# Optimization experiments

Hardware: AMD Instinct MI355X
Metric: run time of the kernel (lower is better)

The kernel has to match this reference:

```python
import jax, jax.numpy as jnp
import numpy as np

N = 100000   # nodes
E = 1000000  # directed edges (before self-loops)
G = 512      # graphs in the batch
NEG_SLOPE = 0.2
EPS = 1e-5


def setup_inputs() -> dict:
    key = jax.random.key(0)
    ks = jax.random.split(key, 24)
    r = lambda i, shape, s=0.1: (jax.random.normal(ks[i], shape) * s).astype(jnp.float32)
    return {
        'x': jax.random.normal(ks[0], (N, 27), dtype=jnp.float32),
        'edge_index': jax.random.randint(ks[1], (2, E), 0, N, dtype=jnp.int32),
        'batch': jnp.sort(jax.random.randint(ks[2], (N,), 0, G, dtype=jnp.int32)),
        # GATv2Conv(26, 32, heads=2)
        'Wl1': r(3, (26, 64)), 'bl1': jnp.zeros(64, jnp.float32),
        'Wr1': r(4, (26, 64)), 'br1': jnp.zeros(64, jnp.float32),
        'att1': r(5, (2, 32)), 'b1': jnp.zeros(64, jnp.float32),
        'g1': jnp.ones(64, jnp.float32), 'be1': jnp.zeros(64, jnp.float32),
        # GATv2Conv(64, 32, heads=1)
        'Wl2': r(6, (64, 32)), 'bl2': jnp.zeros(32, jnp.float32),
        'Wr2': r(7, (64, 32)), 'br2': jnp.zeros(32, jnp.float32),
        'att2': r(8, (1, 32)), 'b2': jnp.zeros(32, jnp.float32),
        'g2': jnp.ones(32, jnp.float32), 'be2': jnp.zeros(32, jnp.float32),
        # gate_nn: 32 -> 16 -> 1
        'Wg1': r(9, (32, 16)), 'bg1': jnp.zeros(16, jnp.float32),
        'Wg2': r(10, (16, 1)), 'bg2': jnp.zeros(1, jnp.float32),
        # final head: 33 -> 16 -> 1
        'Wh1': r(11, (33, 16)), 'bh1': jnp.zeros(16, jnp.float32),
        'Wh2': r(12, (16, 1)), 'bh2': jnp.zeros(1, jnp.float32),
    }


def _gatv2(x, Wl, bl, Wr, br, att, bias, src, dst, heads, ch):
    n = x.shape[0]
    xl = (x @ Wl + bl).reshape(n, heads, ch)  # source projection (messages)
    xr = (x @ Wr + br).reshape(n, heads, ch)  # target projection
    e = jax.nn.leaky_relu(xl[src] + xr[dst], NEG_SLOPE)      # [Etot, H, C]
    logits = jnp.einsum('ehc,hc->eh', e, att)                 # [Etot, H]
    m = jax.ops.segment_max(logits, dst, num_segments=n)
    a = jnp.exp(logits - m[dst])
    z = jax.ops.segment_sum(a, dst, num_segments=n)
    a = a / (z[dst] + 1e-16)
    out = jax.ops.segment_sum(xl[src] * a[:, :, None], dst, num_segments=n)
    return out.reshape(n, heads * ch) + bias


def _batchnorm(h, gamma, beta):
    mu = h.mean(axis=0)
    var = jnp.var(h, axis=0)  # biased, matches torch normalization
    return (h - mu) * jax.lax.rsqrt(var + EPS) * gamma + beta


def reference(x, edge_index, batch, Wl1, bl1, Wr1, br1, att1, b1, g1, be1,
              Wl2, bl2, Wr2, br2, att2, b2, g2, be2,
              Wg1, bg1, Wg2, bg2, Wh1, bh1, Wh2, bh2):
    n = x.shape[0]
    loops = jnp.arange(n, dtype=edge_index.dtype)
    src = jnp.concatenate([edge_index[0], loops])
    dst = jnp.concatenate([edge_index[1], loops])
    x_no_cost = jnp.concatenate([x[:, :24], x[:, 25:]], axis=1)  # [N, 26]
    h = jax.nn.elu(_batchnorm(_gatv2(x_no_cost, Wl1, bl1, Wr1, br1, att1, b1, src, dst, 2, 32), g1, be1))
    # dropout is identity in eval mode
    h = jax.nn.elu(_batchnorm(_gatv2(h, Wl2, bl2, Wr2, br2, att2, b2, src, dst, 1, 32), g2, be2))
    # attentional aggregation: gate MLP + segment softmax over graphs
    gate = jax.nn.relu(h @ Wg1 + bg1) @ Wg2 + bg2               # [N, 1]
    gm = jax.ops.segment_max(gate, batch, num_segments=G)
    ga = jnp.exp(gate - gm[batch])
    gz = jax.ops.segment_sum(ga, batch, num_segments=G)
    ga = ga / (gz[batch] + 1e-16)
    h_pooled = jax.ops.segment_sum(ga * h, batch, num_segments=G)  # [G, 32]
    counts = jax.ops.segment_sum(jnp.ones((n, 1), x.dtype), batch, num_segments=G)
    root_costs = jax.ops.segment_sum(x[:, 24:25], batch, num_segments=G) / jnp.maximum(counts, 1.0)
    combined = jnp.concatenate([h_pooled, root_costs], axis=1)   # [G, 33]
    return jax.nn.relu(combined @ Wh1 + bh1) @ Wh2 + bh2         # [G, 1]
```

## Files before the change

kernel.cpp:

```cpp
#include <hip/hip_runtime.h>
#include <hip/hip_fp16.h>
#include <math.h>

#define NEG 0.2f
#define BN_EPS 1e-5f
#define BKT_W 256
#define CHUNK 4096


__global__ __launch_bounds__(256)
void hist_kernel(const int* __restrict__ ei, int E, int nbh, int nbkt, int* __restrict__ cnt)
{
    __shared__ int hist[512];
    for (int i = threadIdx.x; i < nbkt; i += 256) hist[i] = 0;
    __syncthreads();
    const int g0 = blockIdx.x * (CHUNK / 4);
    #pragma unroll
    for (int it = 0; it < CHUNK / 1024; ++it) {
        int e = (g0 + it * 256 + threadIdx.x) * 4;
        if (e + 3 < E) {
            int4 d4 = *(const int4*)(ei + E + e);
            atomicAdd(&hist[d4.x >> 8], 1);
            atomicAdd(&hist[d4.y >> 8], 1);
            atomicAdd(&hist[d4.z >> 8], 1);
            atomicAdd(&hist[d4.w >> 8], 1);
        } else {
            for (int k = 0; k < 4; ++k)
                if (e + k < E) atomicAdd(&hist[ei[E + e + k] >> 8], 1);
        }
    }
    __syncthreads();
    for (int i = threadIdx.x; i < nbkt; i += 256) cnt[(size_t)i * nbh + blockIdx.x] = hist[i];
}

__global__ __launch_bounds__(256)
void scan_block_kernel(const int* __restrict__ in, int* __restrict__ out,
                       int* __restrict__ bsum, int n)
{
    __shared__ int s[256];
    int i = blockIdx.x * 256 + threadIdx.x;
    int v = (i < n) ? in[i] : 0;
    s[threadIdx.x] = v;
    __syncthreads();
    for (int off = 1; off < 256; off <<= 1) {
        int t = (threadIdx.x >= off) ? s[threadIdx.x - off] : 0;
        __syncthreads();
        s[threadIdx.x] += t;
        __syncthreads();
    }
    if (i < n) out[i + 1] = s[threadIdx.x];
    if (threadIdx.x == 255) bsum[blockIdx.x] = s[255];
}

__global__ __launch_bounds__(512)
void scan_sums_kernel(int* __restrict__ bsum, int nb)
{
    __shared__ int s[512];
    int v = (threadIdx.x < nb) ? bsum[threadIdx.x] : 0;
    s[threadIdx.x] = v;
    __syncthreads();
    for (int off = 1; off < 512; off <<= 1) {
        int t = (threadIdx.x >= off) ? s[threadIdx.x - off] : 0;
        __syncthreads();
        s[threadIdx.x] += t;
        __syncthreads();
    }
    if (threadIdx.x < nb) bsum[threadIdx.x] = s[threadIdx.x] - v;
}

__global__ __launch_bounds__(256)
void scan_add_kernel(int* __restrict__ out, const int* __restrict__ bsum, int n)
{
    int i = blockIdx.x * 256 + threadIdx.x;
    if (i < n) out[i + 1] += bsum[blockIdx.x];
    if (i == 0) out[0] = 0;
}

__global__ __launch_bounds__(256)
void scat_kernel(const int* __restrict__ ei, int E, int nbh, int nbkt,
                 const int* __restrict__ base, int2* __restrict__ pairs)
{
    __shared__ int fill[512];
    __shared__ int lbase[512];
    for (int i = threadIdx.x; i < nbkt; i += 256) {
        fill[i]  = 0;
        lbase[i] = base[(size_t)i * nbh + blockIdx.x];
    }
    __syncthreads();
    const int g0 = blockIdx.x * (CHUNK / 4);
    #pragma unroll
    for (int it = 0; it < CHUNK / 1024; ++it) {
        int e = (g0 + it * 256 + threadIdx.x) * 4;
        if (e + 3 < E) {
            int4 s4 = *(const int4*)(ei + e);
            int4 d4 = *(const int4*)(ei + E + e);
            int b, r;
            b = d4.x >> 8; r = atomicAdd(&fill[b], 1); pairs[lbase[b] + r] = make_int2(s4.x, d4.x);
            b = d4.y >> 8; r = atomicAdd(&fill[b], 1); pairs[lbase[b] + r] = make_int2(s4.y, d4.y);
            b = d4.z >> 8; r = atomicAdd(&fill[b], 1); pairs[lbase[b] + r] = make_int2(s4.z, d4.z);
            b = d4.w >> 8; r = atomicAdd(&fill[b], 1); pairs[lbase[b] + r] = make_int2(s4.w, d4.w);
        } else {
            for (int k = 0; k < 4; ++k) {
                if (e + k < E) {
                    int s = ei[e + k], d = ei[E + e + k];
                    int b = d >> 8;
                    int r = atomicAdd(&fill[b], 1);
                    pairs[lbase[b] + r] = make_int2(s, d);
                }
            }
        }
    }
}

__global__ __launch_bounds__(256)
void bucket_build_kernel(const int2* __restrict__ pairs, const int* __restrict__ base,
                         int nbh, int nbkt, int n, int E,
                         int* __restrict__ rowptr, int* __restrict__ srcs,
                         int* __restrict__ perm)
{
    const int b     = blockIdx.x;
    const int start = base[(size_t)b * nbh];
    const int end   = base[(size_t)(b + 1) * nbh];
    __shared__ int hist[256], sc[256], dcnt[64], dbase[64];
    hist[threadIdx.x] = 0;
    if (threadIdx.x < 64) dcnt[threadIdx.x] = 0;
    __syncthreads();
    for (int j = start + threadIdx.x; j < end; j += 256)
        atomicAdd(&hist[pairs[j].y & 255], 1);
    __syncthreads();
    const int v = hist[threadIdx.x];
    sc[threadIdx.x] = v;
    __syncthreads();
    for (int off = 1; off < 256; off <<= 1) {
        int t = (threadIdx.x >= off) ? sc[threadIdx.x - off] : 0;
        __syncthreads();
        sc[threadIdx.x] += t;
        __syncthreads();
    }
    const int excl = sc[threadIdx.x] - v;
    const int d = b * 256 + threadIdx.x;
    int bin = 0, rnk = 0;
    if (d < n) {
        rowptr[d] = start + excl;
        bin = min(v, 63);
        rnk = atomicAdd(&dcnt[bin], 1);
    }
    if (b == nbkt - 1 && threadIdx.x == 0) rowptr[n] = E;
    __syncthreads();
    hist[threadIdx.x] = excl;
    __syncthreads();
    for (int j = start + threadIdx.x; j < end; j += 256) {
        int2 p = pairs[j];
        int r = atomicAdd(&hist[p.y & 255], 1);
        srcs[start + r] = p.x;
    }
    if (threadIdx.x < 64) dbase[threadIdx.x] = dcnt[threadIdx.x];
    __syncthreads();
    for (int off = 1; off < 64; off <<= 1) {
        int t = 0;
        if (threadIdx.x < 64 && threadIdx.x >= off) t = dbase[threadIdx.x - off];
        __syncthreads();
        if (threadIdx.x < 64) dbase[threadIdx.x] += t;
        __syncthreads();
    }
    if (d < n) perm[b * 256 + (dbase[bin] - dcnt[bin]) + rnk] = d;
}


__device__ __forceinline__ void gat_step4(const uint2 raw, const float* __restrict__ xrv,
                                          const float* __restrict__ at,
                                          float& z, float* __restrict__ acc)
{
    union { uint2 u; __half2 h[2]; } q; q.u = raw;
    const float2 a = __half22float2(q.h[0]);
    const float2 b = __half22float2(q.h[1]);
    float t, p = 0.f;
    t = a.x + xrv[0]; t = t > 0.f ? t : NEG * t; p += t * at[0];
    t = a.y + xrv[1]; t = t > 0.f ? t : NEG * t; p += t * at[1];
    t = b.x + xrv[2]; t = t > 0.f ? t : NEG * t; p += t * at[2];
    t = b.y + xrv[3]; t = t > 0.f ? t : NEG * t; p += t * at[3];
    p += __shfl_xor(p, 1, 64);
    p += __shfl_xor(p, 2, 64);
    p += __shfl_xor(p, 4, 64);
    const float w = __expf(p);
    z += w;
    acc[0] += w * a.x; acc[1] += w * a.y; acc[2] += w * b.x; acc[3] += w * b.y;
}

template<int HC>
__global__ __launch_bounds__(256)
void gat_fused_kernel(const __half* __restrict__ xl, const float* __restrict__ xr,
                      const float* __restrict__ att,
                      const int* __restrict__ rowptr, const int* __restrict__ srcs,
                      const int* __restrict__ perm,
                      float* __restrict__ outp, int n)
{
    constexpr int LPG = HC / 4;
    const int gid  = (blockIdx.x * 256 + threadIdx.x) / LPG;
    const int lane = threadIdx.x % LPG;
    if (gid >= n) return;
    const int d = perm[gid];

    float at[4], xrv[4];
    {
        const float4 a = *(const float4*)(att + lane * 4);
        at[0] = a.x; at[1] = a.y; at[2] = a.z; at[3] = a.w;
        const float4 x0 = *(const float4*)(xr + (size_t)d * HC + lane * 4);
        xrv[0] = x0.x; xrv[1] = x0.y; xrv[2] = x0.z; xrv[3] = x0.w;
    }

    float z = 0.f, acc[4] = {0.f, 0.f, 0.f, 0.f};
    gat_step4(*(const uint2*)(xl + (size_t)d * HC + lane * 4), xrv, at, z, acc);

    const int jb = rowptr[d], je = rowptr[d + 1];
    int j = jb;
    for (; j + 4 <= je; j += 4) {
        const int s0 = srcs[j], s1 = srcs[j + 1], s2 = srcs[j + 2], s3 = srcs[j + 3];
        const uint2 r0 = *(const uint2*)(xl + (size_t)s0 * HC + lane * 4);
        const uint2 r1 = *(const uint2*)(xl + (size_t)s1 * HC + lane * 4);
        const uint2 r2 = *(const uint2*)(xl + (size_t)s2 * HC + lane * 4);
        const uint2 r3 = *(const uint2*)(xl + (size_t)s3 * HC + lane * 4);
        gat_step4(r0, xrv, at, z, acc);
        gat_step4(r1, xrv, at, z, acc);
        gat_step4(r2, xrv, at, z, acc);
        gat_step4(r3, xrv, at, z, acc);
    }
    for (; j < je; ++j)
        gat_step4(*(const uint2*)(xl + (size_t)srcs[j] * HC + lane * 4), xrv, at, z, acc);

    const float inv = 1.f / (z + 1e-16f);
    *(float4*)(outp + (size_t)d * HC + lane * 4) =
        make_float4(acc[0] * inv, acc[1] * inv, acc[2] * inv, acc[3] * inv);
}

template<int K, int OC, bool DROP24, bool FUSE_NORM>
__global__ __launch_bounds__(256)
void proj_kernel(const float* __restrict__ in, int in_stride,
                 const float* __restrict__ Wl, const float* __restrict__ bl,
                 const float* __restrict__ Wr, const float* __restrict__ br,
                 const float* __restrict__ stats, const float* __restrict__ gamma,
                 const float* __restrict__ beta, float inv_n,
                 __half* __restrict__ outl, float* __restrict__ outr, int n)
{
    constexpr int C2  = 2 * OC;
    constexpr int RPI = 256 / C2;
    __shared__ float Wlds[K][C2];
    __shared__ float xs[RPI][K];
    __shared__ float cs[RPI][OC];

    for (int i = threadIdx.x; i < K * OC; i += 256) {
        int k = i / OC, c = i % OC;
        Wlds[k][c]      = Wl[i];
        Wlds[k][OC + c] = Wr[i];
    }
    float na = 1.f, nb = 0.f;
    if constexpr (FUSE_NORM) {
        int kk  = threadIdx.x % K;
        float mu  = stats[kk] * inv_n;
        float var = stats[K + kk] * inv_n - mu * mu;
        float rs  = rsqrtf(var + BN_EPS) * gamma[kk];
        na = rs; nb = beta[kk] - mu * rs;
    }
    __syncthreads();

    const int col  = threadIdx.x % C2;
    const int rloc = threadIdx.x / C2;
    const int rowBase = blockIdx.x * 8;
    const float bias = (col < OC) ? bl[col] : br[col - OC];

    for (int it = 0; it < 8 / RPI; ++it) {
        int row0 = rowBase + it * RPI;
        __syncthreads();
        for (int i = threadIdx.x; i < RPI * K; i += 256) {
            int rr = i / K, k = i % K;
            int row = row0 + rr;
            float v = 0.f;
            if (row < n) {
                if constexpr (DROP24) {
                    int sc = (k < 24) ? k : k + 1;
                    v = in[(size_t)row * in_stride + sc];
                } else {
                    v = in[(size_t)row * in_stride + k];
                }
                if constexpr (FUSE_NORM) {
                    float t = v * na + nb;
                    v = t > 0.f ? t : expm1f(t);
                }
            }
            xs[rr][k] = v;
        }
        __syncthreads();
        int row = row0 + rloc;
        if (row < n) {
            float acc = bias;
            #pragma unroll
            for (int k = 0; k < K; ++k) acc += xs[rloc][k] * Wlds[k][col];
            if (col < OC) cs[rloc][col] = acc;
            else          outr[(size_t)row * OC + (col - OC)] = acc;
        }
        __syncthreads();
        constexpr int NH2 = RPI * OC / 2;
        if (threadIdx.x < NH2) {
            int rr = threadIdx.x / (OC / 2);
            int c  = threadIdx.x % (OC / 2);
            int row2 = row0 + rr;
            if (row2 < n) {
                __half2 hv = __float22half2_rn(make_float2(cs[rr][2 * c], cs[rr][2 * c + 1]));
                *(__half2*)(outl + (size_t)row2 * OC + 2 * c) = hv;
            }
        }
    }
}

template<int C>
__global__ __launch_bounds__(256)
void bn_stats_kernel(const float* __restrict__ h, int n, float* __restrict__ stats)
{
    constexpr int RPB = 256 / C;
    int col = threadIdx.x % C, rg = threadIdx.x / C;
    float s = 0.f, s2 = 0.f;
    for (int r = blockIdx.x * RPB + rg; r < n; r += gridDim.x * RPB) {
        float v = h[(size_t)r * C + col];
        s += v; s2 += v * v;
    }
    __shared__ float red0[256], red1[256];
    red0[threadIdx.x] = s; red1[threadIdx.x] = s2;
    __syncthreads();
    for (int st = 128; st >= C; st >>= 1) {
        if (threadIdx.x < st) {
            red0[threadIdx.x] += red0[threadIdx.x + st];
            red1[threadIdx.x] += red1[threadIdx.x + st];
        }
        __syncthreads();
    }
    if (threadIdx.x < C) {
        atomicAdd(&stats[threadIdx.x],     red0[threadIdx.x]);
        atomicAdd(&stats[C + threadIdx.x], red1[threadIdx.x]);
    }
}

__global__ __launch_bounds__(256)
void gate_norm_kernel(float* __restrict__ h2, int n,
                      const float* __restrict__ stats, const float* __restrict__ gamma,
                      const float* __restrict__ beta, float inv_n,
                      const float* __restrict__ Wg1, const float* __restrict__ bg1,
                      const float* __restrict__ Wg2, const float* __restrict__ bg2,
                      float* __restrict__ gate)
{
    __shared__ float W1[512], W2[16], B1[16], A_[32], B_[32];
    for (int i = threadIdx.x; i < 512; i += 256) W1[i] = Wg1[i];
    if (threadIdx.x < 16) { W2[threadIdx.x] = Wg2[threadIdx.x]; B1[threadIdx.x] = bg1[threadIdx.x]; }
    if (threadIdx.x < 32) {
        float mu  = stats[threadIdx.x] * inv_n;
        float var = stats[32 + threadIdx.x] * inv_n - mu * mu;
        float rs  = rsqrtf(var + BN_EPS) * gamma[threadIdx.x];
        A_[threadIdx.x] = rs;
        B_[threadIdx.x] = beta[threadIdx.x] - mu * rs;
    }
    __syncthreads();
    int node = blockIdx.x * 256 + threadIdx.x;
    if (node >= n) return;
    float* row = h2 + (size_t)node * 32;
    float v[32];
    #pragma unroll
    for (int j = 0; j < 8; ++j) {
        float4 r = *(const float4*)(row + j * 4);
        v[4*j] = r.x; v[4*j+1] = r.y; v[4*j+2] = r.z; v[4*j+3] = r.w;
    }
    #pragma unroll
    for (int k = 0; k < 32; ++k) {
        float t = v[k] * A_[k] + B_[k];
        v[k] = t > 0.f ? t : expm1f(t);
    }
    float hid[16];
    #pragma unroll
    for (int j = 0; j < 16; ++j) hid[j] = B1[j];
    #pragma unroll
    for (int k = 0; k < 32; ++k) {
        #pragma unroll
        for (int j = 0; j < 16; ++j) hid[j] += v[k] * W1[k * 16 + j];
    }
    float g = bg2[0];
    #pragma unroll
    for (int j = 0; j < 16; ++j) g += (hid[j] > 0.f ? hid[j] : 0.f) * W2[j];
    gate[node] = g;
    #pragma unroll
    for (int j = 0; j < 8; ++j)
        *(float4*)(row + j * 4) = make_float4(v[4*j], v[4*j+1], v[4*j+2], v[4*j+3]);
}

__global__ __launch_bounds__(256)
void pool_head_kernel(const float* __restrict__ h2, const float* __restrict__ gate,
                      const int* __restrict__ batch, const float* __restrict__ x,
                      int n, int xstride,
                      const float* __restrict__ Wh1, const float* __restrict__ bh1,
                      const float* __restrict__ Wh2, const float* __restrict__ bh2,
                      float* __restrict__ out)
{
    int g = blockIdx.x;
    __shared__ int sstart, send;
    if (threadIdx.x == 0) {
        int lo = 0, hi = n;
        while (lo < hi) { int mid = (lo + hi) >> 1; if (batch[mid] < g) lo = mid + 1; else hi = mid; }
        sstart = lo;
        hi = n;
        while (lo < hi) { int mid = (lo + hi) >> 1; if (batch[mid] < g + 1) lo = mid + 1; else hi = mid; }
        send = lo;
    }
    __syncthreads();
    const int start = sstart, end = send, cnt = end - start;

    __shared__ float red[256];
    float mx = -INFINITY;
    for (int i = start + threadIdx.x; i < end; i += 256) mx = fmaxf(mx, gate[i]);
    red[threadIdx.x] = mx; __syncthreads();
    for (int st = 128; st > 0; st >>= 1) {
        if (threadIdx.x < st) red[threadIdx.x] = fmaxf(red[threadIdx.x], red[threadIdx.x + st]);
        __syncthreads();
    }
    const float gm = red[0]; __syncthreads();

    float se = 0.f;
    for (int i = start + threadIdx.x; i < end; i += 256) se += expf(gate[i] - gm);
    red[threadIdx.x] = se; __syncthreads();
    for (int st = 128; st > 0; st >>= 1) {
        if (threadIdx.x < st) red[threadIdx.x] += red[threadIdx.x + st];
        __syncthreads();
    }
    const float gz = red[0]; __syncthreads();

    float rc = 0.f;
    for (int i = start + threadIdx.x; i < end; i += 256) rc += x[(size_t)i * xstride + 24];
    red[threadIdx.x] = rc; __syncthreads();
    for (int st = 128; st > 0; st >>= 1) {
        if (threadIdx.x < st) red[threadIdx.x] += red[threadIdx.x + st];
        __syncthreads();
    }
    const float root = red[0] / fmaxf((float)cnt, 1.f); __syncthreads();

    const int col = threadIdx.x % 32, rg = threadIdx.x / 32;
    float acc = 0.f;
    for (int i = start + rg; i < end; i += 8) acc += expf(gate[i] - gm) * h2[(size_t)i * 32 + col];
    red[threadIdx.x] = acc; __syncthreads();
    for (int st = 128; st >= 32; st >>= 1) {
        if (threadIdx.x < st) red[threadIdx.x] += red[threadIdx.x + st];
        __syncthreads();
    }
    __shared__ float comb[33];
    if (threadIdx.x < 32) comb[threadIdx.x] = red[threadIdx.x] / (gz + 1e-16f);
    if (threadIdx.x == 0) comb[32] = root;
    __syncthreads();

    __shared__ float hidr[16];
    if (threadIdx.x < 16) {
        float hv = bh1[threadIdx.x];
        #pragma unroll
        for (int k = 0; k < 33; ++k) hv += comb[k] * Wh1[k * 16 + threadIdx.x];
        hidr[threadIdx.x] = hv > 0.f ? hv : 0.f;
    }
    __syncthreads();
    if (threadIdx.x == 0) {
        float r = bh2[0];
        #pragma unroll
        for (int j = 0; j < 16; ++j) r += hidr[j] * Wh2[j];
        out[g] = r;
    }
}


extern "C" void kernel_launch(void* const* d_in, const int* in_sizes, int n_in,
                              void* d_out, int out_size, void* d_ws, size_t ws_size,
                              hipStream_t stream)
{
    const float* x    = (const float*)d_in[0];
    const int*   ei   = (const int*)d_in[1];
    const int*   batch= (const int*)d_in[2];
    const float* Wl1  = (const float*)d_in[3];
    const float* bl1  = (const float*)d_in[4];
    const float* Wr1  = (const float*)d_in[5];
    const float* br1  = (const float*)d_in[6];
    const float* att1 = (const float*)d_in[7];
    const float* g1   = (const float*)d_in[9];
    const float* be1  = (const float*)d_in[10];
    const float* Wl2  = (const float*)d_in[11];
    const float* bl2  = (const float*)d_in[12];
    const float* Wr2  = (const float*)d_in[13];
    const float* br2  = (const float*)d_in[14];
    const float* att2 = (const float*)d_in[15];
    const float* g2   = (const float*)d_in[17];
    const float* be2  = (const float*)d_in[18];
    const float* Wg1  = (const float*)d_in[19];
    const float* bg1  = (const float*)d_in[20];
    const float* Wg2  = (const float*)d_in[21];
    const float* bg2  = (const float*)d_in[22];
    const float* Wh1  = (const float*)d_in[23];
    const float* bh1  = (const float*)d_in[24];
    const float* Wh2  = (const float*)d_in[25];
    const float* bh2  = (const float*)d_in[26];

    const int n  = in_sizes[0] / 27;
    const int E  = in_sizes[1] / 2;
    const int G  = out_size;
    const float inv_n = 1.f / (float)n;

    const int nbkt = (n + BKT_W - 1) / BKT_W;
    const int nbh  = (E + CHUNK - 1) / CHUNK;
    const int SZ   = nbkt * nbh;
    const int NBs  = (SZ + 255) / 256;

    float* ws = (float*)d_ws;
    size_t off = 0;
    auto align4 = [&](size_t v) { return (v + 3) & ~(size_t)3; };
    float* st1 = ws + off; off += 128;
    float* st2 = ws + off; off += 64;
    const size_t zero_floats = off;
    int* cnt     = (int*)(ws + off); off = align4(off + SZ);
    int* basearr = (int*)(ws + off); off = align4(off + SZ + 1);
    int* bsum    = (int*)(ws + off); off = align4(off + 512);
    int* rowptr  = (int*)(ws + off); off = align4(off + n + 1);
    int* srcs    = (int*)(ws + off); off = align4(off + E);
    int* perm    = (int*)(ws + off); off = align4(off + n);
    __half* xl1h = (__half*)(ws + off); off += (size_t)n * 32;
    float* xr1   = ws + off; off += (size_t)n * 64;
    float* h1    = ws + off; off += (size_t)n * 64;
    float* h2    = ws + off; off += (size_t)n * 32;
    int2* pairs   = (int2*)h1;
    __half* xl2h  = xl1h;
    float* xr2    = xr1;
    float* gate   = xr1 + (size_t)n * 32;

    hipMemsetAsync(d_ws, 0, zero_floats * sizeof(float), stream);

    hist_kernel<<<nbh, 256, 0, stream>>>(ei, E, nbh, nbkt, cnt);
    scan_block_kernel<<<NBs, 256, 0, stream>>>(cnt, basearr, bsum, SZ);
    scan_sums_kernel<<<1, 512, 0, stream>>>(bsum, NBs);
    scan_add_kernel<<<NBs, 256, 0, stream>>>(basearr, bsum, SZ);
    scat_kernel<<<nbh, 256, 0, stream>>>(ei, E, nbh, nbkt, basearr, pairs);
    bucket_build_kernel<<<nbkt, 256, 0, stream>>>(pairs, basearr, nbh, nbkt, n, E, rowptr, srcs, perm);

    proj_kernel<26, 64, true, false><<<(n + 7) / 8, 256, 0, stream>>>(
        x, 27, Wl1, bl1, Wr1, br1, nullptr, nullptr, nullptr, 0.f, xl1h, xr1, n);
    gat_fused_kernel<64><<<(n * 16 + 255) / 256, 256, 0, stream>>>(
        xl1h, xr1, att1, rowptr, srcs, perm, h1, n);
    bn_stats_kernel<64><<<256, 256, 0, stream>>>(h1, n, st1);

    proj_kernel<64, 32, false, true><<<(n + 7) / 8, 256, 0, stream>>>(
        h1, 64, Wl2, bl2, Wr2, br2, st1, g1, be1, inv_n, xl2h, xr2, n);
    gat_fused_kernel<32><<<(n * 8 + 255) / 256, 256, 0, stream>>>(
        xl2h, xr2, att2, rowptr, srcs, perm, h2, n);
    bn_stats_kernel<32><<<256, 256, 0, stream>>>(h2, n, st2);

    gate_norm_kernel<<<(n + 255) / 256, 256, 0, stream>>>(
        h2, n, st2, g2, be2, inv_n, Wg1, bg1, Wg2, bg2, gate);
    pool_head_kernel<<<G, 256, 0, stream>>>(h2, gate, batch, x, n, 27, Wh1, bh1, Wh2, bh2, (float*)d_out);
}
```

Measured before the change: 306.5 us.

## Register-block projection kernel over larger row tiles with weights held in registers

The projection kernel now stages a larger tile of input rows (32 or 64) in shared memory with one barrier and keeps each thread's weight column in registers. Each thread computes several output rows, so the weight load is amortized and the per-iteration barriers and the half-precision staging buffer go away. Left outputs are now written as individual halves instead of packed half2, which may make those stores less coalesced. Register pressure rises for K=64, and the grid has fewer blocks.

```diff
diff --git a/kernel.cpp b/kernel.cpp
--- a/kernel.cpp
+++ b/kernel.cpp
@@ -233,7 +233,7 @@
         make_float4(acc[0] * inv, acc[1] * inv, acc[2] * inv, acc[3] * inv);
 }
 
-template<int K, int OC, bool DROP24, bool FUSE_NORM>
+template<int K, int OC, bool DROP24, bool FUSE_NORM, int TR>
 __global__ __launch_bounds__(256)
 void proj_kernel(const float* __restrict__ in, int in_stride,
                  const float* __restrict__ Wl, const float* __restrict__ bl,
@@ -242,17 +242,19 @@
                  const float* __restrict__ beta, float inv_n,
                  __half* __restrict__ outl, float* __restrict__ outr, int n)
 {
-    constexpr int C2  = 2 * OC;
-    constexpr int RPI = 256 / C2;
+    constexpr int C2    = 2 * OC;
+    constexpr int RSTEP = 256 / C2;
+    constexpr int NR    = TR / RSTEP;
+    constexpr int XLD   = (K % 4) ? (K + 4 - (K % 4)) : K;
     __shared__ float Wlds[K][C2];
-    __shared__ float xs[RPI][K];
-    __shared__ float cs[RPI][OC];
+    __shared__ float xs[TR][XLD];
 
     for (int i = threadIdx.x; i < K * OC; i += 256) {
         int k = i / OC, c = i % OC;
         Wlds[k][c]      = Wl[i];
         Wlds[k][OC + c] = Wr[i];
     }
+
     float na = 1.f, nb = 0.f;
     if constexpr (FUSE_NORM) {
         int kk  = threadIdx.x % K;
@@ -261,53 +263,46 @@
         float rs  = rsqrtf(var + BN_EPS) * gamma[kk];
         na = rs; nb = beta[kk] - mu * rs;
     }
-    __syncthreads();
-
-    const int col  = threadIdx.x % C2;
-    const int rloc = threadIdx.x / C2;
-    const int rowBase = blockIdx.x * 8;
-    const float bias = (col < OC) ? bl[col] : br[col - OC];
-
-    for (int it = 0; it < 8 / RPI; ++it) {
-        int row0 = rowBase + it * RPI;
-        __syncthreads();
-        for (int i = threadIdx.x; i < RPI * K; i += 256) {
-            int rr = i / K, k = i % K;
-            int row = row0 + rr;
-            float v = 0.f;
-            if (row < n) {
-                if constexpr (DROP24) {
-                    int sc = (k < 24) ? k : k + 1;
-                    v = in[(size_t)row * in_stride + sc];
-                } else {
-                    v = in[(size_t)row * in_stride + k];
-                }
-                if constexpr (FUSE_NORM) {
-                    float t = v * na + nb;
-                    v = t > 0.f ? t : expm1f(t);
-                }
+
+    const int row0 = blockIdx.x * TR;
+    for (int i = threadIdx.x; i < TR * K; i += 256) {
+        int r = i / K, k = i % K;
+        int row = row0 + r;
+        float v = 0.f;
+        if (row < n) {
+            int sc = DROP24 ? (k < 24 ? k : k + 1) : k;
+            v = in[(size_t)row * in_stride + sc];
+            if constexpr (FUSE_NORM) {
+                float t = v * na + nb;
+                v = t > 0.f ? t : expm1f(t);
             }
-            xs[rr][k] = v;
         }
-        __syncthreads();
-        int row = row0 + rloc;
+        xs[r][k] = v;
+    }
+    __syncthreads();
+
+    const int c  = threadIdx.x % C2;
+    const int rr = threadIdx.x / C2;
+    float w[K];
+    #pragma unroll
+    for (int k = 0; k < K; ++k) w[k] = Wlds[k][c];
+    const float bias = (c < OC) ? bl[c] : br[c - OC];
+
+    float acc[NR];
+    #pragma unroll
+    for (int ri = 0; ri < NR; ++ri) {
+        const float* xrow = xs[rr + ri * RSTEP];
+        float a = bias;
+        #pragma unroll
+        for (int k = 0; k < K; ++k) a += xrow[k] * w[k];
+        acc[ri] = a;
+    }
+    #pragma unroll
+    for (int ri = 0; ri < NR; ++ri) {
+        int row = row0 + rr + ri * RSTEP;
         if (row < n) {
-            float acc = bias;
-            #pragma unroll
-            for (int k = 0; k < K; ++k) acc += xs[rloc][k] * Wlds[k][col];
-            if (col < OC) cs[rloc][col] = acc;
-            else          outr[(size_t)row * OC + (col - OC)] = acc;
-        }
-        __syncthreads();
-        constexpr int NH2 = RPI * OC / 2;
-        if (threadIdx.x < NH2) {
-            int rr = threadIdx.x / (OC / 2);
-            int c  = threadIdx.x % (OC / 2);
-            int row2 = row0 + rr;
-            if (row2 < n) {
-                __half2 hv = __float22half2_rn(make_float2(cs[rr][2 * c], cs[rr][2 * c + 1]));
-                *(__half2*)(outl + (size_t)row2 * OC + 2 * c) = hv;
-            }
+            if (c < OC) outl[(size_t)row * OC + c] = __float2half(acc[ri]);
+            else        outr[(size_t)row * OC + (c - OC)] = acc[ri];
         }
     }
 }
@@ -538,13 +533,13 @@
     scat_kernel<<<nbh, 256, 0, stream>>>(ei, E, nbh, nbkt, basearr, pairs);
     bucket_build_kernel<<<nbkt, 256, 0, stream>>>(pairs, basearr, nbh, nbkt, n, E, rowptr, srcs, perm);
 
-    proj_kernel<26, 64, true, false><<<(n + 7) / 8, 256, 0, stream>>>(
+    proj_kernel<26, 64, true, false, 32><<<(n + 31) / 32, 256, 0, stream>>>(
         x, 27, Wl1, bl1, Wr1, br1, nullptr, nullptr, nullptr, 0.f, xl1h, xr1, n);
     gat_fused_kernel<64><<<(n * 16 + 255) / 256, 256, 0, stream>>>(
         xl1h, xr1, att1, rowptr, srcs, perm, h1, n);
     bn_stats_kernel<64><<<256, 256, 0, stream>>>(h1, n, st1);
 
-    proj_kernel<64, 32, false, true><<<(n + 7) / 8, 256, 0, stream>>>(
+    proj_kernel<64, 32, false, true, 64><<<(n + 63) / 64, 256, 0, stream>>>(
         h1, 64, Wl2, bl2, Wr2, br2, st1, g1, be1, inv_n, xl2h, xr2, n);
     gat_fused_kernel<32><<<(n * 8 + 255) / 256, 256, 0, stream>>>(
         xl2h, xr2, att2, rowptr, srcs, perm, h2, n);
```

Result: slower. 776.3 us (+153.3%).
